# Kernel optimization log

Measured on AMD Instinct MI355X. Metric: run time of the kernel, lower is better.

Reference implementation:

```python
import jax, jax.numpy as jnp
import numpy as np

B, Z, D, V, IN, R = 4, 128, 2, 2, 512, 256


def setup_inputs() -> dict:
    key = jax.random.key(0)
    ks = jax.random.split(key, 9)
    scale = 1.0 / np.sqrt(IN)
    inp = {
        "x1": jax.random.normal(ks[0], (B, Z, D, V, IN), jnp.float32),
        "x2": jax.random.normal(ks[1], (B, Z, D, V, IN), jnp.float32),
        "x3": jax.random.normal(ks[2], (B, Z, D, V, IN), jnp.float32),
        "W1": jax.random.normal(ks[3], (IN, R), jnp.float32) * scale,
        "b1": jax.random.normal(ks[4], (R,), jnp.float32) * scale,
        "W2": jax.random.normal(ks[5], (IN, R), jnp.float32) * scale,
        "b2": jax.random.normal(ks[6], (R,), jnp.float32) * scale,
        "W3": jax.random.normal(ks[7], (IN, R), jnp.float32) * scale,
        "b3": jax.random.normal(ks[8], (R,), jnp.float32) * scale,
    }
    return inp


def reference(x1, x2, x3, W1, b1, W2, b2, W3, b3):
    # Linear projections: [b, pos, d, v, in] @ [in, r] -> [b, pos, d, v, r]
    p1 = jnp.einsum('bzdvi,ir->bzdvr', x1, W1) + b1
    p2 = jnp.einsum('bxdvi,ir->bxdvr', x2, W2) + b2
    p3 = jnp.einsum('bcdvi,ir->bcdvr', x3, W3) + b3
    # Trilinear contraction over the factorized rank r, broadcasting over d, v
    return jnp.einsum('bzdve,bxdve,bcdve->bzxcdv', p1, p2, p3)
```

## Files before the change

kernel.cpp:

```cpp
#include <hip/hip_runtime.h>
#include <hip/hip_bf16.h>


typedef _Float16 f16;
typedef __attribute__((ext_vector_type(8)))  _Float16 f16x8;
typedef __attribute__((ext_vector_type(4)))  float    f32x4;
typedef __attribute__((ext_vector_type(16))) float    f32x16;

__device__ __forceinline__ void lds_barrier() {
    __builtin_amdgcn_sched_barrier(0);
    asm volatile("s_waitcnt lgkmcnt(0)" ::: "memory");
    __builtin_amdgcn_s_barrier();
    __builtin_amdgcn_sched_barrier(0);
}

__global__ __launch_bounds__(128) void proj_kernel(
    const float* __restrict__ x1, const float* __restrict__ x2, const float* __restrict__ x3,
    const float* __restrict__ W1, const float* __restrict__ b1,
    const float* __restrict__ W2, const float* __restrict__ b2,
    const float* __restrict__ W3, const float* __restrict__ b3,
    f16* __restrict__ p1, f16* __restrict__ p2, f16* __restrict__ p3) {
    const int mat = blockIdx.z;
    const float* __restrict__ x    = (mat == 0) ? x1 : (mat == 1) ? x2 : x3;
    const float* __restrict__ W    = (mat == 0) ? W1 : (mat == 1) ? W2 : W3;
    const float* __restrict__ bias = (mat == 0) ? b1 : (mat == 1) ? b2 : b3;
    f16* __restrict__ p = (mat == 0) ? p1 : (mat == 1) ? p2 : p3;

    const int tid  = threadIdx.x;
    const int lane = tid & 63;
    const int w    = tid >> 6;
    const int ln   = lane & 31;
    const int kq   = lane >> 5;
    const int m0   = blockIdx.x * 64 + w * 32;
    const int n0b  = blockIdx.y * 32;

    __shared__ f16 sWt[2][32 * 40];

    f32x16 acc;
#pragma unroll
    for (int i = 0; i < 16; ++i) acc[i] = 0.f;

    const int snn = tid & 31, skk0 = tid >> 5;
    const float* Xr = x + (size_t)(m0 + ln) * 512 + kq * 8;

    float wr[8], wr2[8];
    f32x4 xr[4], xn[4];
#pragma unroll
    for (int j = 0; j < 8; ++j)
        wr[j] = W[(size_t)(skk0 + 4 * j) * 256 + n0b + snn];
#pragma unroll
    for (int t = 0; t < 2; ++t) {
        xr[2 * t]     = *(const f32x4*)(Xr + t * 16);
        xr[2 * t + 1] = *(const f32x4*)(Xr + t * 16 + 4);
    }

#pragma unroll 1
    for (int ch = 0; ch < 16; ++ch) {
        const int buf = ch & 1;
#pragma unroll
        for (int j = 0; j < 8; ++j)
            sWt[buf][snn * 40 + skk0 + 4 * j] = (f16)wr[j];
        if (ch < 15) {
            const int k1 = (ch + 1) * 32;
#pragma unroll
            for (int j = 0; j < 8; ++j)
                wr2[j] = W[(size_t)(k1 + skk0 + 4 * j) * 256 + n0b + snn];
#pragma unroll
            for (int t = 0; t < 2; ++t) {
                xn[2 * t]     = *(const f32x4*)(Xr + k1 + t * 16);
                xn[2 * t + 1] = *(const f32x4*)(Xr + k1 + t * 16 + 4);
            }
        }
        lds_barrier();
#pragma unroll
        for (int ks = 0; ks < 2; ++ks) {
            f32x4 a0 = xr[2 * ks], a1 = xr[2 * ks + 1];
            f16x8 av;
            av[0] = (f16)a0[0]; av[1] = (f16)a0[1]; av[2] = (f16)a0[2]; av[3] = (f16)a0[3];
            av[4] = (f16)a1[0]; av[5] = (f16)a1[1]; av[6] = (f16)a1[2]; av[7] = (f16)a1[3];
            f16x8 bv = *(const f16x8*)&sWt[buf][ln * 40 + ks * 16 + kq * 8];
            acc = __builtin_amdgcn_mfma_f32_32x32x16_f16(av, bv, acc, 0, 0, 0);
        }
#pragma unroll
        for (int t = 0; t < 4; ++t) xr[t] = xn[t];
#pragma unroll
        for (int j = 0; j < 8; ++j) wr[j] = wr2[j];
    }

    const int n = n0b + ln;
    const float bn = bias[n];
#pragma unroll
    for (int i = 0; i < 16; ++i) {
        const int m  = m0 + (i & 3) + 8 * (i >> 2) + 4 * kq;
        const int bb = m >> 9, z = (m >> 2) & 127, dv = m & 3;
        p[((bb * 4 + dv) * 128 + z) * 256 + n] = (f16)(acc[i] + bn);
    }
}

__global__ __launch_bounds__(256, 2) void tri_kernel(
    const f16* __restrict__ p1, const f16* __restrict__ p2,
    const f16* __restrict__ p3, float* __restrict__ out) {
    const int bi = blockIdx.x;
    const int zg = bi & 15;
    const int ct = (bi >> 4) & 3;
    const int xt = (bi >> 6) & 3;
    const int b  = bi >> 8;

    const int tid  = threadIdx.x;
    const int lane = tid & 63;
    const int w    = tid >> 6;
    const int ln   = lane & 31;
    const int kq   = lane >> 5;
    const int x0   = xt * 32;
    const int c0   = ct * 32;
    const int z0   = zg * 8;
    const int sl   = b * 4 + w;

    __shared__ __align__(16) f16  sP1[4][8 * 256];
    __shared__ float sT[2][4 * 32 * 33];

#pragma unroll
    for (int i = 0; i < 4; ++i) {
        const int G  = i * 64 + lane;
        const int zo = G >> 5, es = G & 31;
        f16x8 v = *(const f16x8*)(p1 + ((sl * 128 + z0 + zo) << 8) + es * 8);
        *(f16x8*)&sP1[w][G * 8] = v;
    }

    f16x8 pv[16], bq[16];
    const f16* P2r = p2 + ((sl * 128 + x0 + ln) << 8) + kq * 8;
    const f16* P3r = p3 + ((sl * 128 + c0 + ln) << 8) + kq * 8;
#pragma unroll
    for (int ks = 0; ks < 16; ++ks) {
        pv[ks] = *(const f16x8*)(P2r + ks * 16);
        bq[ks] = *(const f16x8*)(P3r + ks * 16);
    }

    const int cl = tid & 31, xg = tid >> 5;

#pragma unroll 1
    for (int zi = 0; zi < 8; ++zi) {
        f32x16 acc;
#pragma unroll
        for (int i = 0; i < 16; ++i) acc[i] = 0.f;

#pragma unroll
        for (int ks = 0; ks < 16; ++ks) {
            f16x8 u = *(const f16x8*)&sP1[w][(zi * 32 + ks * 2 + kq) * 8];
            f16x8 af = u * pv[ks];
            acc = __builtin_amdgcn_mfma_f32_32x32x16_f16(af, bq[ks], acc, 0, 0, 0);
        }

        float* T = sT[zi & 1];
#pragma unroll
        for (int i = 0; i < 16; ++i) {
            const int xl = (i & 3) + 8 * (i >> 2) + 4 * kq;
            T[w * 1056 + xl * 33 + ln] = acc[i];
        }
        lds_barrier();

        const int z = z0 + zi;
#pragma unroll
        for (int j = 0; j < 4; ++j) {
            const int xl = xg * 4 + j;
            f32x4 v;
            v[0] = T[0 * 1056 + xl * 33 + cl];
            v[1] = T[1 * 1056 + xl * 33 + cl];
            v[2] = T[2 * 1056 + xl * 33 + cl];
            v[3] = T[3 * 1056 + xl * 33 + cl];
            const size_t idx = (size_t)((b * 128 + z) * 128 + x0 + xl) * 128 + c0 + cl;
            *(f32x4*)(out + idx * 4) = v;
        }
    }
}

extern "C" void kernel_launch(void* const* d_in, const int* in_sizes, int n_in,
                              void* d_out, int out_size, void* d_ws, size_t ws_size,
                              hipStream_t stream) {
    const float* x1 = (const float*)d_in[0];
    const float* x2 = (const float*)d_in[1];
    const float* x3 = (const float*)d_in[2];
    const float* W1 = (const float*)d_in[3];
    const float* b1 = (const float*)d_in[4];
    const float* W2 = (const float*)d_in[5];
    const float* b2 = (const float*)d_in[6];
    const float* W3 = (const float*)d_in[7];
    const float* b3 = (const float*)d_in[8];

    char* ws = (char*)d_ws;
    f16* p1 = (f16*)ws;
    f16* p2 = (f16*)(ws + (1u << 20));
    f16* p3 = (f16*)(ws + 2u * (1u << 20));

    proj_kernel<<<dim3(32, 8, 3), 128, 0, stream>>>(x1, x2, x3, W1, b1, W2, b2, W3, b3,
                                                    p1, p2, p3);
    tri_kernel<<<dim3(1024), 256, 0, stream>>>(p1, p2, p3, (float*)d_out);
}
```

Before: 53.02 us.

## Overlap output stores of previous z slice with MFMA compute of current slice

Software-pipelines the per-z loop in the trilinear kernel. The previous slice's transposed results are read from the other LDS buffer and written to global memory in between the MFMA steps for the current slice, with a peeled prologue and epilogue. The aim is to hide the global store latency and LDS reads behind matrix compute instead of running them in series after each barrier. In exchange, the loop has more code and register pressure may rise under the two-waves-per-SIMD launch bound.

```diff
diff --git a/kernel.cpp b/kernel.cpp
--- a/kernel.cpp
+++ b/kernel.cpp
@@ -138,8 +138,30 @@
 
     const int cl = tid & 31, xg = tid >> 5;
 
+    {
+        f32x16 acc;
+#pragma unroll
+        for (int i = 0; i < 16; ++i) acc[i] = 0.f;
+#pragma unroll
+        for (int ks = 0; ks < 16; ++ks) {
+            f16x8 u = *(const f16x8*)&sP1[w][(ks * 2 + kq) * 8];
+            f16x8 af = u * pv[ks];
+            acc = __builtin_amdgcn_mfma_f32_32x32x16_f16(af, bq[ks], acc, 0, 0, 0);
+        }
+        float* T = sT[0];
+#pragma unroll
+        for (int i = 0; i < 16; ++i) {
+            const int xl = (i & 3) + 8 * (i >> 2) + 4 * kq;
+            T[w * 1056 + xl * 33 + ln] = acc[i];
+        }
+        lds_barrier();
+    }
+
 #pragma unroll 1
-    for (int zi = 0; zi < 8; ++zi) {
+    for (int zi = 1; zi < 8; ++zi) {
+        const float* P = sT[(zi - 1) & 1];
+        float*       T = sT[zi & 1];
+        const int zprev = z0 + zi - 1;
         f32x16 acc;
 #pragma unroll
         for (int i = 0; i < 16; ++i) acc[i] = 0.f;
@@ -149,26 +171,37 @@
             f16x8 u = *(const f16x8*)&sP1[w][(zi * 32 + ks * 2 + kq) * 8];
             f16x8 af = u * pv[ks];
             acc = __builtin_amdgcn_mfma_f32_32x32x16_f16(af, bq[ks], acc, 0, 0, 0);
-        }
-
-        float* T = sT[zi & 1];
+            if ((ks & 3) == 0) {
+                const int j  = ks >> 2;
+                const int xl = xg * 4 + j;
+                f32x4 v;
+                v[0] = P[0 * 1056 + xl * 33 + cl];
+                v[1] = P[1 * 1056 + xl * 33 + cl];
+                v[2] = P[2 * 1056 + xl * 33 + cl];
+                v[3] = P[3 * 1056 + xl * 33 + cl];
+                const size_t idx = (size_t)((b * 128 + zprev) * 128 + x0 + xl) * 128 + c0 + cl;
+                *(f32x4*)(out + idx * 4) = v;
+            }
+        }
 #pragma unroll
         for (int i = 0; i < 16; ++i) {
             const int xl = (i & 3) + 8 * (i >> 2) + 4 * kq;
             T[w * 1056 + xl * 33 + ln] = acc[i];
         }
         lds_barrier();
-
-        const int z = z0 + zi;
+    }
+
+    {
+        const float* P = sT[1];
 #pragma unroll
         for (int j = 0; j < 4; ++j) {
             const int xl = xg * 4 + j;
             f32x4 v;
-            v[0] = T[0 * 1056 + xl * 33 + cl];
-            v[1] = T[1 * 1056 + xl * 33 + cl];
-            v[2] = T[2 * 1056 + xl * 33 + cl];
-            v[3] = T[3 * 1056 + xl * 33 + cl];
-            const size_t idx = (size_t)((b * 128 + z) * 128 + x0 + xl) * 128 + c0 + cl;
+            v[0] = P[0 * 1056 + xl * 33 + cl];
+            v[1] = P[1 * 1056 + xl * 33 + cl];
+            v[2] = P[2 * 1056 + xl * 33 + cl];
+            v[3] = P[3 * 1056 + xl * 33 + cl];
+            const size_t idx = (size_t)((b * 128 + z0 + 7) * 128 + x0 + xl) * 128 + c0 + cl;
             *(f32x4*)(out + idx * 4) = v;
         }
     }
```

New measurement: 59.44 us. 12.1% more time.
